# Optimization experiments

Hardware: AMD Instinct MI355X
Metric: run time of the kernel (lower is better)

The kernel has to match this reference:

```python
import jax, jax.numpy as jnp
import numpy as np

HIDDEN = 3072
N_HEADS = 16
Q_LORA = 1536
KV_LORA = 512
NOPE = 128
ROPE = 64
QK_HD = NOPE + ROPE  # 192
V_HD = 128
B, S = 2, 1024


def rms_norm(x, w, eps=1e-6):
    xf = x.astype(jnp.float32)
    var = jnp.mean(xf * xf, axis=-1, keepdims=True)
    return w * (xf * jax.lax.rsqrt(var + eps)).astype(x.dtype)


def apply_rope(x):
    # x: (b, s, h, d) with d even; interleaved pair rotation as in the source
    b, s, h, d = x.shape
    pos = jnp.arange(s, dtype=jnp.float32)
    inv_freq = 1.0 / (10000.0 ** (jnp.arange(0, d, 2, dtype=jnp.float32) / d))
    ang = pos[:, None] * inv_freq[None, :]          # (s, d/2)
    sin = jnp.sin(ang)[None, :, None, :]            # (1, s, 1, d/2)
    cos = jnp.cos(ang)[None, :, None, :]
    xr = x.reshape(b, s, h, d // 2, 2)
    x1, x2 = xr[..., 0], xr[..., 1]
    r1 = x1 * cos - x2 * sin
    r2 = x1 * sin + x2 * cos
    return jnp.stack([r1, r2], axis=-1).reshape(b, s, h, d)


def setup_inputs() -> dict:
    key = jax.random.key(0)
    ks = jax.random.split(key, 16)
    sc = 0.02
    inp = {
        "hidden_states": jax.random.normal(ks[0], (B, S, HIDDEN), jnp.float32),
        # causal additive mask (s, t): 0 on/below diagonal, -1e9 above
        "mask": jnp.where(jnp.tril(jnp.ones((S, S), bool)), 0.0, -1e9).astype(jnp.float32),
        "wq_a_w": jax.random.normal(ks[1], (Q_LORA, HIDDEN), jnp.float32) * sc,
        "wq_a_b": jnp.zeros((Q_LORA,), jnp.float32),
        "q_norm_w": jnp.ones((Q_LORA,), jnp.float32),
        "wq_b_w": jax.random.normal(ks[2], (HIDDEN, Q_LORA), jnp.float32) * sc,
        "wq_b_b": jnp.zeros((HIDDEN,), jnp.float32),
        "wkv_a_w": jax.random.normal(ks[3], (KV_LORA + ROPE, HIDDEN), jnp.float32) * sc,
        "wkv_a_b": jnp.zeros((KV_LORA + ROPE,), jnp.float32),
        "kv_norm_w": jnp.ones((KV_LORA,), jnp.float32),
        "wkv_b_w": jax.random.normal(ks[4], (N_HEADS * (NOPE + V_HD), KV_LORA), jnp.float32) * sc,
        "wkv_b_b": jnp.zeros((N_HEADS * (NOPE + V_HD),), jnp.float32),
        "wo_w": jax.random.normal(ks[5], (HIDDEN, N_HEADS * V_HD), jnp.float32) * sc,
        "wo_b": jnp.zeros((HIDDEN,), jnp.float32),
    }
    return inp


def reference(hidden_states, mask, wq_a_w, wq_a_b, q_norm_w, wq_b_w, wq_b_b,
              wkv_a_w, wkv_a_b, kv_norm_w, wkv_b_w, wkv_b_b, wo_w, wo_b):
    b, s, _ = hidden_states.shape
    scale = QK_HD ** (-0.5)

    # low-rank Q projection
    q_lat = hidden_states @ wq_a_w.T + wq_a_b                  # (b,s,q_lora)
    q = rms_norm(q_lat, q_norm_w) @ wq_b_w.T + wq_b_b          # (b,s,hidden)
    q = q.reshape(b, s, N_HEADS, QK_HD)
    q_nope, q_rope = q[..., :NOPE], q[..., NOPE:]
    q_rope = apply_rope(q_rope)
    q = jnp.concatenate([q_nope, q_rope], axis=-1)             # (b,s,h,192)

    # low-rank KV projection with decoupled rope key
    kv = hidden_states @ wkv_a_w.T + wkv_a_b                   # (b,s,kv_lora+rope)
    kv_lat, k_rope = kv[..., :KV_LORA], kv[..., KV_LORA:]
    k_rope = apply_rope(k_rope[:, :, None, :])                 # (b,s,1,64)
    kv = rms_norm(kv_lat, kv_norm_w) @ wkv_b_w.T + wkv_b_b
    kv = kv.reshape(b, s, N_HEADS, NOPE + V_HD)
    k_nope, v = kv[..., :NOPE], kv[..., NOPE:]
    k = jnp.concatenate([k_nope, jnp.broadcast_to(k_rope, (b, s, N_HEADS, ROPE))], axis=-1)

    # naive full attention, fp32 softmax (as in source)
    scores = jnp.einsum('bshd,bthd->bsht', q, k) * scale       # (b,s,h,t)
    scores = scores + mask[None, :, None, :]
    p = jax.nn.softmax(scores.astype(jnp.float32), axis=-1)
    out = jnp.einsum('bsht,bthd->bshd', p, v)                  # (b,s,h,v_hd)
    out = out.reshape(b, s, N_HEADS * V_HD)
    return out @ wo_w.T + wo_b
```

## Files before the change

kernel.cpp:

```cpp
#include <hip/hip_runtime.h>
#include <stdint.h>
#include <stddef.h>

#define NHEADS 16
#define QLORA  1536
#define KVLORA 512
#define QKH    192
#define VH     128
#define BB     2
#define SS     1024
#define MROWS  (BB*SS)
#define HID    3072

typedef __attribute__((ext_vector_type(4))) float fx4;
typedef __attribute__((ext_vector_type(4))) short sx4;
typedef __attribute__((ext_vector_type(8))) short sx8;

__device__ __forceinline__ short f2bf(float f) {
  uint32_t u = __builtin_bit_cast(uint32_t, f);
  u = (u + 0x7fffu + ((u >> 16) & 1u)) >> 16;
  return (short)u;
}
__device__ __forceinline__ float bf2f(short s) {
  uint32_t u = ((uint32_t)(uint16_t)s) << 16;
  return __builtin_bit_cast(float, u);
}
__device__ __forceinline__ void gl_lds16(const void* g, void* l) {
  __builtin_amdgcn_global_load_lds((const __attribute__((address_space(1))) void*)g,
                                   (__attribute__((address_space(3))) void*)l, 16, 0, 0);
}
__device__ __forceinline__ sx8 ldfrag(const short* p) {
  sx4 lo = *(const sx4*)p;
  sx4 hi = *(const sx4*)(p + 16);
  sx8 r;
  r[0]=lo[0]; r[1]=lo[1]; r[2]=lo[2]; r[3]=lo[3];
  r[4]=hi[0]; r[5]=hi[1]; r[6]=hi[2]; r[7]=hi[3];
  return r;
}
__device__ __forceinline__ sx8 ldfrag_swz(const short* lds, int row, int rowShorts,
                                          int baseChunk, int g) {
  const int r7 = row & 7;
  const int gh = g >> 1, lo4 = (g & 1) * 4;
  int ch0 = baseChunk + gh;
  int ch1 = baseChunk + 2 + gh;
  ch0 = (ch0 & ~7) | ((ch0 & 7) ^ r7);
  ch1 = (ch1 & ~7) | ((ch1 & 7) ^ r7);
  const short* base = lds + row * rowShorts;
  sx4 a = *(const sx4*)(base + ch0 * 8 + lo4);
  sx4 b = *(const sx4*)(base + ch1 * 8 + lo4);
  sx8 r;
  r[0]=a[0]; r[1]=a[1]; r[2]=a[2]; r[3]=a[3];
  r[4]=b[0]; r[5]=b[1]; r[6]=b[2]; r[7]=b[3];
  return r;
}

struct CvtSeg { const float* src; short* dst; int n4; };
__global__ void k_cvt6(CvtSeg s0, CvtSeg s1, CvtSeg s2, CvtSeg s3, CvtSeg s4, CvtSeg s5) {
  const CvtSeg segs[6] = {s0, s1, s2, s3, s4, s5};
  const int stride = gridDim.x * blockDim.x;
  const int t0 = blockIdx.x * blockDim.x + threadIdx.x;
#pragma unroll
  for (int s = 0; s < 6; ++s) {
    const float* src = segs[s].src;
    short* dst = segs[s].dst;
    const int n4 = segs[s].n4;
    for (int i = t0; i < n4; i += stride) {
      fx4 v = *(const fx4*)(src + (size_t)i * 4);
      sx4 o;
      o[0] = f2bf(v[0]); o[1] = f2bf(v[1]); o[2] = f2bf(v[2]); o[3] = f2bf(v[3]);
      *(sx4*)(dst + (size_t)i * 4) = o;
    }
  }
}

__global__ void k_rope_tab(float* __restrict__ tab) {
  int i = blockIdx.x * blockDim.x + threadIdx.x;
  if (i >= SS * 32) return;
  int pos = i >> 5, fi = i & 31;
  float inv = powf(10000.0f, -(float)fi / 32.0f);
  float ang = (float)pos * inv;
  tab[i * 2]     = cosf(ang);
  tab[i * 2 + 1] = sinf(ang);
}

struct GemmProb {
  const short* A; const short* Bt; const float* bias; void* C;
  int N; int K;
};

template <int MFR, int SPLITK>
__global__ __launch_bounds__(256, 2)
void k_gemmS(GemmProb p0, GemmProb p1, int nblk0) {
  constexpr int TM = MFR * 32;
  constexpr int MT = 2048 / TM;
  int nwg = gridDim.x;
  int bid = (blockIdx.x % 8) * (nwg >> 3) + (blockIdx.x >> 3);
  const GemmProb p = (bid < nblk0) ? p0 : p1;
  int lb = (bid < nblk0) ? bid : bid - nblk0;
  const int N = p.N, K = p.K;
  const int NT = (N + 127) >> 7;
  const int tiles = MT * NT;
  const int tile = lb % tiles;
  const int pi = (SPLITK > 1) ? (lb / tiles) : 0;
  const int m0 = (tile % MT) * TM;
  const int n0 = (tile / MT) * 128;
  const int Kc = K / SPLITK;
  const int k0 = pi * Kc;

  __shared__ short As[TM * 64];
  __shared__ short Bs[128 * 64];
  const int tid  = threadIdx.x;
  const int lane = tid & 63;
  const int g    = lane >> 4;
  const int r16  = lane & 15;
  const int wave = tid >> 6;
  const int wm   = (wave >> 1) * (TM / 2);
  const int wn   = (wave & 1) * 64;

  fx4 acc[MFR][4] = {};

  for (int kk = k0; kk < k0 + Kc; kk += 64) {
#pragma unroll
    for (int i = 0; i < MFR; ++i) {
      int cc  = tid + 256 * i;
      int row = cc >> 3;
      int src = ((cc & 7) ^ (row & 7)) * 8;
      gl_lds16(p.A + (size_t)(m0 + row) * K + kk + src, &As[cc * 8]);
    }
#pragma unroll
    for (int i = 0; i < 4; ++i) {
      int cc  = tid + 256 * i;
      int row = cc >> 3;
      int src = ((cc & 7) ^ (row & 7)) * 8;
      int bn = n0 + row; if (bn > N - 1) bn = N - 1;
      gl_lds16(p.Bt + (size_t)bn * K + kk + src, &Bs[cc * 8]);
    }
    __syncthreads();

#pragma unroll
    for (int s = 0; s < 2; ++s) {
      sx8 bfv[4];
#pragma unroll
      for (int ni = 0; ni < 4; ++ni)
        bfv[ni] = ldfrag_swz(Bs, wn + ni * 16 + r16, 64, s * 4, g);
#pragma unroll
      for (int mi = 0; mi < MFR; ++mi) {
        sx8 af = ldfrag_swz(As, wm + mi * 16 + r16, 64, s * 4, g);
#pragma unroll
        for (int ni = 0; ni < 4; ++ni)
          acc[mi][ni] = __builtin_amdgcn_mfma_f32_16x16x32_bf16(af, bfv[ni], acc[mi][ni], 0, 0, 0);
      }
    }
    __syncthreads();
  }

  if (SPLITK > 1) {
    float* Cp = (float*)p.C + (size_t)pi * 2048 * N;
#pragma unroll
    for (int mi = 0; mi < MFR; ++mi) {
      int mbase = m0 + wm + mi * 16 + 4 * g;
#pragma unroll
      for (int ni = 0; ni < 4; ++ni) {
        int ncol = n0 + wn + ni * 16 + r16;
        if (ncol < N) {
#pragma unroll
          for (int r = 0; r < 4; ++r)
            Cp[(size_t)(mbase + r) * N + ncol] = acc[mi][ni][r];
        }
      }
    }
  } else {
#pragma unroll
    for (int mi = 0; mi < MFR; ++mi) {
      int mbase = m0 + wm + mi * 16 + 4 * g;
#pragma unroll
      for (int ni = 0; ni < 4; ++ni) {
        int ncol = n0 + wn + ni * 16 + r16;
        if (ncol < N) {
          float bv = p.bias[ncol];
#pragma unroll
          for (int r = 0; r < 4; ++r)
            ((short*)p.C)[(size_t)(mbase + r) * N + ncol] = f2bf(acc[mi][ni][r] + bv);
        }
      }
    }
  }
}

__global__ __launch_bounds__(256)
void k_prep(const float* __restrict__ qp, const float* __restrict__ q_bias,
            const float* __restrict__ q_norm_w, short* __restrict__ qn,
            const float* __restrict__ kvp, const float* __restrict__ kv_bias,
            const float* __restrict__ kv_norm_w, short* __restrict__ kvn,
            short* __restrict__ kr, const float* __restrict__ tab) {
  const int row = blockIdx.x;
  const int t = threadIdx.x;
  const size_t QS = (size_t)2048 * QLORA;
  const size_t KS = (size_t)2048 * 576;

  float x[8];
  float s1 = 0.f, s2 = 0.f;
  if (t < 192) {
    const float* a = qp + (size_t)row * QLORA + t * 8;
    fx4 u0 = *(const fx4*)(a),          u1 = *(const fx4*)(a + 4);
    fx4 v0 = *(const fx4*)(a + QS),     v1 = *(const fx4*)(a + QS + 4);
    fx4 w0 = *(const fx4*)(a + 2 * QS), w1 = *(const fx4*)(a + 2 * QS + 4);
#pragma unroll
    for (int j = 0; j < 4; ++j) {
      x[j]     = u0[j] + v0[j] + w0[j] + q_bias[t * 8 + j];
      x[4 + j] = u1[j] + v1[j] + w1[j] + q_bias[t * 8 + 4 + j];
    }
#pragma unroll
    for (int j = 0; j < 8; ++j) s1 += x[j] * x[j];
  } else {
    const int c = t - 192;
    const float* a = kvp + (size_t)row * 576 + c * 8;
    fx4 u0 = *(const fx4*)(a),          u1 = *(const fx4*)(a + 4);
    fx4 v0 = *(const fx4*)(a + KS),     v1 = *(const fx4*)(a + KS + 4);
    fx4 w0 = *(const fx4*)(a + 2 * KS), w1 = *(const fx4*)(a + 2 * KS + 4);
#pragma unroll
    for (int j = 0; j < 4; ++j) {
      x[j]     = u0[j] + v0[j] + w0[j] + kv_bias[c * 8 + j];
      x[4 + j] = u1[j] + v1[j] + w1[j] + kv_bias[c * 8 + 4 + j];
    }
#pragma unroll
    for (int j = 0; j < 8; ++j) s2 += x[j] * x[j];
  }
#pragma unroll
  for (int o = 32; o >= 1; o >>= 1) {
    s1 += __shfl_xor(s1, o, 64);
    s2 += __shfl_xor(s2, o, 64);
  }
  __shared__ float r1[4], r2[4];
  if ((t & 63) == 0) { r1[t >> 6] = s1; r2[t >> 6] = s2; }
  __syncthreads();
  float qss = r1[0] + r1[1] + r1[2] + r1[3];
  float kss = r2[0] + r2[1] + r2[2] + r2[3];
  float qrs = 1.0f / sqrtf(qss / (float)QLORA + 1e-6f);
  float krs = 1.0f / sqrtf(kss / (float)KVLORA + 1e-6f);

  if (t < 192) {
    sx8 o;
#pragma unroll
    for (int j = 0; j < 8; ++j) o[j] = f2bf(x[j] * qrs * q_norm_w[t * 8 + j]);
    *(sx8*)(qn + (size_t)row * QLORA + t * 8) = o;
  } else {
    int c = t - 192;
    sx8 o;
#pragma unroll
    for (int j = 0; j < 8; ++j) o[j] = f2bf(x[j] * krs * kv_norm_w[c * 8 + j]);
    *(sx8*)(kvn + (size_t)row * KVLORA + c * 8) = o;
  }
  if (t < 8) {
    const float* a = kvp + (size_t)row * 576 + 512 + t * 8;
    fx4 u0 = *(const fx4*)(a),          u1 = *(const fx4*)(a + 4);
    fx4 v0 = *(const fx4*)(a + KS),     v1 = *(const fx4*)(a + KS + 4);
    fx4 w0 = *(const fx4*)(a + 2 * KS), w1 = *(const fx4*)(a + 2 * KS + 4);
    float y[8];
#pragma unroll
    for (int j = 0; j < 4; ++j) {
      y[j]     = u0[j] + v0[j] + w0[j] + kv_bias[512 + t * 8 + j];
      y[4 + j] = u1[j] + v1[j] + w1[j] + kv_bias[512 + t * 8 + 4 + j];
    }
    int pos = row & (SS - 1);
    sx8 o;
#pragma unroll
    for (int k = 0; k < 4; ++k) {
      int i = t * 4 + k;
      float c = tab[(pos * 32 + i) * 2], s = tab[(pos * 32 + i) * 2 + 1];
      o[2 * k]     = f2bf(y[2 * k] * c - y[2 * k + 1] * s);
      o[2 * k + 1] = f2bf(y[2 * k] * s + y[2 * k + 1] * c);
    }
    *(sx8*)(kr + (size_t)row * 64 + t * 8) = o;
  }
}

__global__ __launch_bounds__(256)
void k_post(const short* __restrict__ kvb, short* __restrict__ vt,
            short* __restrict__ qb, const float* __restrict__ tab) {
  const int bid = blockIdx.x;
  const int tid = threadIdx.x;
  if (bid < 512) {
    const int bh = bid >> 4;
    const int t0 = (bid & 15) * 64;
    const int b = bh >> 4, h = bh & 15;
    __shared__ short sm[64 * 128];
#pragma unroll
    for (int i = 0; i < 4; ++i) {
      int c = tid + 256 * i;
      int tt = c >> 4, d0 = (c & 15) * 8;
      sx8 v = *(const sx8*)(kvb + ((size_t)(b * SS + t0 + tt)) * 4096 + h * 256 + 128 + d0);
      *(sx8*)(sm + tt * 128 + d0) = v;
    }
    __syncthreads();
#pragma unroll
    for (int i = 0; i < 4; ++i) {
      int c = tid + 256 * i;
      int d = c >> 3, tof = (c & 7) * 8;
      sx8 v;
#pragma unroll
      for (int j = 0; j < 8; ++j) v[j] = sm[(tof + j) * 128 + d];
      *(sx8*)(vt + ((size_t)bh * VH + d) * SS + t0 + tof) = v;
    }
  } else {
    int p = (bid - 512) * 256 + tid;
    int j = p & 7, h = (p >> 3) & 15, row = p >> 7;
    int pos = row & (SS - 1);
    size_t base = (((size_t)row * NHEADS + h) * QKH) + 128 + j * 8;
    sx8 x = *(const sx8*)(qb + base);
    sx8 o;
#pragma unroll
    for (int k = 0; k < 4; ++k) {
      int i = j * 4 + k;
      float c = tab[(pos * 32 + i) * 2], s = tab[(pos * 32 + i) * 2 + 1];
      float x1 = bf2f(x[2 * k]), x2 = bf2f(x[2 * k + 1]);
      o[2 * k]     = f2bf(x1 * c - x2 * s);
      o[2 * k + 1] = f2bf(x1 * s + x2 * c);
    }
    *(sx8*)(qb + base) = o;
  }
}

__global__ __launch_bounds__(256)
void k_osum(const float* __restrict__ p, const float* __restrict__ bias,
            float* __restrict__ out) {
  const size_t OS = (size_t)2048 * HID;
  int i = blockIdx.x * 256 + threadIdx.x;
  fx4 a = *(const fx4*)(p + (size_t)i * 4);
  fx4 b = *(const fx4*)(p + OS + (size_t)i * 4);
  int col = (i * 4) % HID;
  fx4 bv = *(const fx4*)(bias + col);
  fx4 o = a + b + bv;
  *(fx4*)(out + (size_t)i * 4) = o;
}

__global__ __launch_bounds__(256, 2)
void k_attn(const short* __restrict__ q, const short* __restrict__ kvb,
            const short* __restrict__ kr, const short* __restrict__ vt,
            short* __restrict__ ao) {
  const int bh = blockIdx.x;
  const int b = bh >> 4, h = bh & 15;
  const int qt0 = blockIdx.y * 64;
  const int tid = threadIdx.x;
  const int lane = tid & 63;
  const int wave = tid >> 6;
  const int g = lane >> 4, r16 = lane & 15;
  const int qg = qt0 + wave * 16 + r16;

  __shared__ short Ks[64 * QKH];
  __shared__ short Vs[VH * 64];

  sx8 qf[6];
  {
    const short* qr = q + (((size_t)(b * SS + qg)) * NHEADS + h) * QKH;
#pragma unroll
    for (int f = 0; f < 6; ++f) qf[f] = ldfrag(qr + f * 32 + 4 * g);
  }

  float mrun = -1e30f, lrun = 0.0f;
  fx4 oacc[8] = {};
  const float scale = 0.07216878364870323f;

  const int ntiles = qt0 / 64 + 1;
  for (int kt = 0; kt < ntiles; ++kt) {
    const int t0 = kt * 64;
#pragma unroll
    for (int i = 0; i < 6; ++i) {
      int cc = tid + 256 * i;
      int row = cc / 24, ch = cc % 24;
      int sc = (ch & 24) | ((ch & 7) ^ (row & 7));
      size_t grow = (size_t)(b * SS + t0 + row);
      const short* src = (sc < 16) ? kvb + grow * 4096 + h * 256 + sc * 8
                                   : kr + grow * 64 + (sc - 16) * 8;
      gl_lds16(src, &Ks[cc * 8]);
    }
#pragma unroll
    for (int i = 0; i < 4; ++i) {
      int cc = tid + 256 * i;
      int row = cc >> 3;
      int sc = (cc & 7) ^ (row & 7);
      gl_lds16(vt + ((size_t)bh * VH + row) * SS + t0 + sc * 8, &Vs[cc * 8]);
    }
    __syncthreads();

    const bool diag = (kt == ntiles - 1);
    float pv[16];
    float tmax = -1e30f;
#pragma unroll
    for (int th = 0; th < 4; ++th) {
      fx4 sacc = {};
#pragma unroll
      for (int f = 0; f < 6; ++f) {
        sx8 kf = ldfrag_swz(Ks, th * 16 + r16, QKH, f * 4, g);
        sacc = __builtin_amdgcn_mfma_f32_16x16x32_bf16(kf, qf[f], sacc, 0, 0, 0);
      }
#pragma unroll
      for (int r = 0; r < 4; ++r) {
        int t = t0 + th * 16 + 4 * g + r;
        float s = sacc[r] * scale;
        if (diag && t > qg) s = -1e30f;
        pv[th * 4 + r] = s;
        tmax = fmaxf(tmax, s);
      }
    }
    tmax = fmaxf(tmax, __shfl_xor(tmax, 16, 64));
    tmax = fmaxf(tmax, __shfl_xor(tmax, 32, 64));
    float mnew = fmaxf(mrun, tmax);
    float corr = __expf(mrun - mnew);
    float psum = 0.f;
#pragma unroll
    for (int j = 0; j < 16; ++j) { pv[j] = __expf(pv[j] - mnew); psum += pv[j]; }
    psum += __shfl_xor(psum, 16, 64);
    psum += __shfl_xor(psum, 32, 64);
    lrun = lrun * corr + psum;
    mrun = mnew;
#pragma unroll
    for (int f8 = 0; f8 < 8; ++f8) oacc[f8] *= corr;

    sx8 pf0, pf1;
#pragma unroll
    for (int j = 0; j < 8; ++j) { pf0[j] = f2bf(pv[j]); pf1[j] = f2bf(pv[8 + j]); }

#pragma unroll
    for (int f8 = 0; f8 < 8; ++f8) {
      sx8 v0 = ldfrag_swz(Vs, f8 * 16 + r16, 64, 0, g);
      sx8 v1 = ldfrag_swz(Vs, f8 * 16 + r16, 64, 4, g);
      oacc[f8] = __builtin_amdgcn_mfma_f32_16x16x32_bf16(v0, pf0, oacc[f8], 0, 0, 0);
      oacc[f8] = __builtin_amdgcn_mfma_f32_16x16x32_bf16(v1, pf1, oacc[f8], 0, 0, 0);
    }
    __syncthreads();
  }

  float inv = 1.0f / lrun;
#pragma unroll
  for (int f8 = 0; f8 < 8; ++f8)
#pragma unroll
    for (int r = 0; r < 4; ++r) {
      int d = f8 * 16 + 4 * g + r;
      ao[(((size_t)(b * SS + qg)) * NHEADS + h) * VH + d] = f2bf(oacc[f8][r] * inv);
    }
}

extern "C" void kernel_launch(void* const* d_in, const int* in_sizes, int n_in,
                              void* d_out, int out_size, void* d_ws, size_t ws_size,
                              hipStream_t stream) {
  const float* hs       = (const float*)d_in[0];
  const float* wq_a_w   = (const float*)d_in[2];
  const float* wq_a_b   = (const float*)d_in[3];
  const float* q_norm_w = (const float*)d_in[4];
  const float* wq_b_w   = (const float*)d_in[5];
  const float* wq_b_b   = (const float*)d_in[6];
  const float* wkv_a_w  = (const float*)d_in[7];
  const float* wkv_a_b  = (const float*)d_in[8];
  const float* kv_norm_w= (const float*)d_in[9];
  const float* wkv_b_w  = (const float*)d_in[10];
  const float* wkv_b_b  = (const float*)d_in[11];
  const float* wo_w     = (const float*)d_in[12];
  const float* wo_b     = (const float*)d_in[13];
  float* out = (float*)d_out;

  short* ws0 = (short*)d_ws;
  size_t off = 0;
  short* wqa_bf  = ws0 + off; off += (size_t)QLORA * HID;
  short* wqb_bf  = ws0 + off; off += (size_t)HID * QLORA;
  short* wkva_bf = ws0 + off; off += (size_t)576 * HID;
  short* wkvb_bf = ws0 + off; off += (size_t)4096 * KVLORA;
  short* wo_bf   = ws0 + off; off += (size_t)HID * 2048;
  short* h_bf    = ws0 + off; off += (size_t)MROWS * HID;
  short* qn      = ws0 + off; off += (size_t)MROWS * QLORA;
  short* kvn     = ws0 + off; off += (size_t)MROWS * KVLORA;
  short* kr      = ws0 + off; off += (size_t)MROWS * 64;
  short* qb      = ws0 + off; off += (size_t)MROWS * HID;
  short* kvb     = ws0 + off; off += (size_t)MROWS * 4096;
  short* vtb     = ws0 + off; off += (size_t)BB * NHEADS * VH * SS;
  short* ao      = ws0 + off; off += (size_t)MROWS * 2048;
  float* tab     = (float*)(ws0 + off + (off & 1));
  float* arena   = tab + SS * 64;
  float* qlatp   = arena;
  float* kvp     = arena + (size_t)3 * 2048 * QLORA;
  float* wop     = arena;

  {
    CvtSeg s0{wq_a_w,  wqa_bf,  (int)((size_t)QLORA * HID / 4)};
    CvtSeg s1{wq_b_w,  wqb_bf,  (int)((size_t)HID * QLORA / 4)};
    CvtSeg s2{wkv_a_w, wkva_bf, (int)((size_t)576 * HID / 4)};
    CvtSeg s3{wkv_b_w, wkvb_bf, (int)((size_t)4096 * KVLORA / 4)};
    CvtSeg s4{wo_w,    wo_bf,   (int)((size_t)HID * 2048 / 4)};
    CvtSeg s5{hs,      h_bf,    (int)((size_t)MROWS * HID / 4)};
    k_cvt6<<<2048, 256, 0, stream>>>(s0, s1, s2, s3, s4, s5);
  }
  k_rope_tab<<<(SS * 32 + 255) / 256, 256, 0, stream>>>(tab);

  {
    GemmProb pq{h_bf, wqa_bf,  nullptr, qlatp, QLORA, HID};
    GemmProb pk{h_bf, wkva_bf, nullptr, kvp,   576,   HID};
    int nb0 = 8 * (QLORA / 128) * 3;
    int nb1 = 8 * ((576 + 127) / 128) * 3;
    k_gemmS<8, 3><<<nb0 + nb1, 256, 0, stream>>>(pq, pk, nb0);
  }

  k_prep<<<MROWS, 256, 0, stream>>>(qlatp, wq_a_b, q_norm_w, qn,
                                    kvp, wkv_a_b, kv_norm_w, kvn, kr, tab);

  {
    GemmProb pq{qn,  wqb_bf,  wq_b_b,  qb,  HID,  QLORA};
    GemmProb pk{kvn, wkvb_bf, wkv_b_b, kvb, 4096, KVLORA};
    int nb0 = 8 * (HID / 128);
    int nb1 = 8 * (4096 / 128);
    k_gemmS<8, 1><<<nb0 + nb1, 256, 0, stream>>>(pq, pk, nb0);
  }

  k_post<<<512 + 1024, 256, 0, stream>>>(kvb, vtb, qb, tab);

  k_attn<<<dim3(BB * NHEADS, SS / 64), 256, 0, stream>>>(qb, kvb, kr, vtb, ao);

  {
    GemmProb po{ao, wo_bf, nullptr, wop, HID, 2048};
    int nb = 8 * (HID / 128) * 2;
    k_gemmS<8, 2><<<nb, 256, 0, stream>>>(po, po, nb);
  }
  k_osum<<<(MROWS * HID / 4) / 256, 256, 0, stream>>>(wop, wo_b, out);
}
```

Measured before the change: 244.1 us.

## Overlap weight conversion with GEMMs, bf16 split-K partials, balance causal attention tiles

The conversion kernel now handles only the hidden states and the first-stage weights, and it also builds the rope table, which removes one launch. The remaining weight conversions run in 192 extra blocks appended to the earlier GEMM launches, so they overlap with matrix work. Split-K partial sums are stored as bf16 instead of fp32, halving partial-sum traffic at some cost in accuracy. The attention query-tile order is remapped to pair short and long causal tiles for better load balance.

```diff
diff --git a/kernel.cpp b/kernel.cpp
--- a/kernel.cpp
+++ b/kernel.cpp
@@ -55,32 +55,31 @@
 }
 
 struct CvtSeg { const float* src; short* dst; int n4; };
-__global__ void k_cvt6(CvtSeg s0, CvtSeg s1, CvtSeg s2, CvtSeg s3, CvtSeg s4, CvtSeg s5) {
-  const CvtSeg segs[6] = {s0, s1, s2, s3, s4, s5};
-  const int stride = gridDim.x * blockDim.x;
-  const int t0 = blockIdx.x * blockDim.x + threadIdx.x;
-#pragma unroll
-  for (int s = 0; s < 6; ++s) {
-    const float* src = segs[s].src;
-    short* dst = segs[s].dst;
-    const int n4 = segs[s].n4;
-    for (int i = t0; i < n4; i += stride) {
-      fx4 v = *(const fx4*)(src + (size_t)i * 4);
-      sx4 o;
-      o[0] = f2bf(v[0]); o[1] = f2bf(v[1]); o[2] = f2bf(v[2]); o[3] = f2bf(v[3]);
-      *(sx4*)(dst + (size_t)i * 4) = o;
-    }
-  }
-}
-
-__global__ void k_rope_tab(float* __restrict__ tab) {
-  int i = blockIdx.x * blockDim.x + threadIdx.x;
-  if (i >= SS * 32) return;
-  int pos = i >> 5, fi = i & 31;
-  float inv = powf(10000.0f, -(float)fi / 32.0f);
-  float ang = (float)pos * inv;
-  tab[i * 2]     = cosf(ang);
-  tab[i * 2 + 1] = sinf(ang);
+__device__ __forceinline__ void cvt_one(const CvtSeg& sg, int i) {
+  fx4 v = *(const fx4*)(sg.src + (size_t)i * 4);
+  sx4 o;
+  o[0] = f2bf(v[0]); o[1] = f2bf(v[1]); o[2] = f2bf(v[2]); o[3] = f2bf(v[3]);
+  *(sx4*)(sg.dst + (size_t)i * 4) = o;
+}
+
+__global__ void k_cvt3(CvtSeg s0, CvtSeg s1, CvtSeg s2, float* __restrict__ tab) {
+  if ((int)blockIdx.x >= 1024) {
+    int i = ((int)blockIdx.x - 1024) * 256 + threadIdx.x;
+    if (i < SS * 32) {
+      int pos = i >> 5, fi = i & 31;
+      float inv = powf(10000.0f, -(float)fi / 32.0f);
+      float ang = (float)pos * inv;
+      tab[i * 2]     = cosf(ang);
+      tab[i * 2 + 1] = sinf(ang);
+    }
+    return;
+  }
+  const CvtSeg segs[3] = {s0, s1, s2};
+  const int stride = 1024 * 256;
+  const int t0 = blockIdx.x * 256 + threadIdx.x;
+#pragma unroll
+  for (int s = 0; s < 3; ++s)
+    for (int i = t0; i < segs[s].n4; i += stride) cvt_one(segs[s], i);
 }
 
 struct GemmProb {
@@ -90,11 +89,18 @@
 
 template <int MFR, int SPLITK>
 __global__ __launch_bounds__(256, 2)
-void k_gemmS(GemmProb p0, GemmProb p1, int nblk0) {
+void k_gemmS(GemmProb p0, GemmProb p1, int nblk0, int nbGemm,
+             CvtSeg c0, CvtSeg c1) {
+  if ((int)blockIdx.x >= nbGemm) {
+    const int nthr = ((int)gridDim.x - nbGemm) * 256;
+    const int t0 = ((int)blockIdx.x - nbGemm) * 256 + threadIdx.x;
+    if (c0.src) for (int i = t0; i < c0.n4; i += nthr) cvt_one(c0, i);
+    if (c1.src) for (int i = t0; i < c1.n4; i += nthr) cvt_one(c1, i);
+    return;
+  }
   constexpr int TM = MFR * 32;
   constexpr int MT = 2048 / TM;
-  int nwg = gridDim.x;
-  int bid = (blockIdx.x % 8) * (nwg >> 3) + (blockIdx.x >> 3);
+  int bid = ((int)blockIdx.x % 8) * (nbGemm >> 3) + ((int)blockIdx.x >> 3);
   const GemmProb p = (bid < nblk0) ? p0 : p1;
   int lb = (bid < nblk0) ? bid : bid - nblk0;
   const int N = p.N, K = p.K;
@@ -155,7 +161,7 @@
   }
 
   if (SPLITK > 1) {
-    float* Cp = (float*)p.C + (size_t)pi * 2048 * N;
+    short* Cp = (short*)p.C + (size_t)pi * 2048 * N;
 #pragma unroll
     for (int mi = 0; mi < MFR; ++mi) {
       int mbase = m0 + wm + mi * 16 + 4 * g;
@@ -165,7 +171,7 @@
         if (ncol < N) {
 #pragma unroll
           for (int r = 0; r < 4; ++r)
-            Cp[(size_t)(mbase + r) * N + ncol] = acc[mi][ni][r];
+            Cp[(size_t)(mbase + r) * N + ncol] = f2bf(acc[mi][ni][r]);
         }
       }
     }
@@ -188,9 +194,9 @@
 }
 
 __global__ __launch_bounds__(256)
-void k_prep(const float* __restrict__ qp, const float* __restrict__ q_bias,
+void k_prep(const short* __restrict__ qp, const float* __restrict__ q_bias,
             const float* __restrict__ q_norm_w, short* __restrict__ qn,
-            const float* __restrict__ kvp, const float* __restrict__ kv_bias,
+            const short* __restrict__ kvp, const float* __restrict__ kv_bias,
             const float* __restrict__ kv_norm_w, short* __restrict__ kvn,
             short* __restrict__ kr, const float* __restrict__ tab) {
   const int row = blockIdx.x;
@@ -201,30 +207,26 @@
   float x[8];
   float s1 = 0.f, s2 = 0.f;
   if (t < 192) {
-    const float* a = qp + (size_t)row * QLORA + t * 8;
-    fx4 u0 = *(const fx4*)(a),          u1 = *(const fx4*)(a + 4);
-    fx4 v0 = *(const fx4*)(a + QS),     v1 = *(const fx4*)(a + QS + 4);
-    fx4 w0 = *(const fx4*)(a + 2 * QS), w1 = *(const fx4*)(a + 2 * QS + 4);
-#pragma unroll
-    for (int j = 0; j < 4; ++j) {
-      x[j]     = u0[j] + v0[j] + w0[j] + q_bias[t * 8 + j];
-      x[4 + j] = u1[j] + v1[j] + w1[j] + q_bias[t * 8 + 4 + j];
-    }
-#pragma unroll
-    for (int j = 0; j < 8; ++j) s1 += x[j] * x[j];
+    const short* a = qp + (size_t)row * QLORA + t * 8;
+    sx8 u = *(const sx8*)(a);
+    sx8 v = *(const sx8*)(a + QS);
+    sx8 w = *(const sx8*)(a + 2 * QS);
+#pragma unroll
+    for (int j = 0; j < 8; ++j) {
+      x[j] = bf2f(u[j]) + bf2f(v[j]) + bf2f(w[j]) + q_bias[t * 8 + j];
+      s1 += x[j] * x[j];
+    }
   } else {
     const int c = t - 192;
-    const float* a = kvp + (size_t)row * 576 + c * 8;
-    fx4 u0 = *(const fx4*)(a),          u1 = *(const fx4*)(a + 4);
-    fx4 v0 = *(const fx4*)(a + KS),     v1 = *(const fx4*)(a + KS + 4);
-    fx4 w0 = *(const fx4*)(a + 2 * KS), w1 = *(const fx4*)(a + 2 * KS + 4);
-#pragma unroll
-    for (int j = 0; j < 4; ++j) {
-      x[j]     = u0[j] + v0[j] + w0[j] + kv_bias[c * 8 + j];
-      x[4 + j] = u1[j] + v1[j] + w1[j] + kv_bias[c * 8 + 4 + j];
-    }
-#pragma unroll
-    for (int j = 0; j < 8; ++j) s2 += x[j] * x[j];
+    const short* a = kvp + (size_t)row * 576 + c * 8;
+    sx8 u = *(const sx8*)(a);
+    sx8 v = *(const sx8*)(a + KS);
+    sx8 w = *(const sx8*)(a + 2 * KS);
+#pragma unroll
+    for (int j = 0; j < 8; ++j) {
+      x[j] = bf2f(u[j]) + bf2f(v[j]) + bf2f(w[j]) + kv_bias[c * 8 + j];
+      s2 += x[j] * x[j];
+    }
   }
 #pragma unroll
   for (int o = 32; o >= 1; o >>= 1) {
@@ -252,16 +254,14 @@
     *(sx8*)(kvn + (size_t)row * KVLORA + c * 8) = o;
   }
   if (t < 8) {
-    const float* a = kvp + (size_t)row * 576 + 512 + t * 8;
-    fx4 u0 = *(const fx4*)(a),          u1 = *(const fx4*)(a + 4);
-    fx4 v0 = *(const fx4*)(a + KS),     v1 = *(const fx4*)(a + KS + 4);
-    fx4 w0 = *(const fx4*)(a + 2 * KS), w1 = *(const fx4*)(a + 2 * KS + 4);
+    const short* a = kvp + (size_t)row * 576 + 512 + t * 8;
+    sx8 u = *(const sx8*)(a);
+    sx8 v = *(const sx8*)(a + KS);
+    sx8 w = *(const sx8*)(a + 2 * KS);
     float y[8];
 #pragma unroll
-    for (int j = 0; j < 4; ++j) {
-      y[j]     = u0[j] + v0[j] + w0[j] + kv_bias[512 + t * 8 + j];
-      y[4 + j] = u1[j] + v1[j] + w1[j] + kv_bias[512 + t * 8 + 4 + j];
-    }
+    for (int j = 0; j < 8; ++j)
+      y[j] = bf2f(u[j]) + bf2f(v[j]) + bf2f(w[j]) + kv_bias[512 + t * 8 + j];
     int pos = row & (SS - 1);
     sx8 o;
 #pragma unroll
@@ -322,16 +322,21 @@
 }
 
 __global__ __launch_bounds__(256)
-void k_osum(const float* __restrict__ p, const float* __restrict__ bias,
+void k_osum(const short* __restrict__ p, const float* __restrict__ bias,
             float* __restrict__ out) {
   const size_t OS = (size_t)2048 * HID;
   int i = blockIdx.x * 256 + threadIdx.x;
-  fx4 a = *(const fx4*)(p + (size_t)i * 4);
-  fx4 b = *(const fx4*)(p + OS + (size_t)i * 4);
-  int col = (i * 4) % HID;
-  fx4 bv = *(const fx4*)(bias + col);
-  fx4 o = a + b + bv;
-  *(fx4*)(out + (size_t)i * 4) = o;
+  sx8 a = *(const sx8*)(p + (size_t)i * 8);
+  sx8 b = *(const sx8*)(p + OS + (size_t)i * 8);
+  int col = (i * 8) % HID;
+  fx4 o0, o1;
+#pragma unroll
+  for (int j = 0; j < 4; ++j) {
+    o0[j] = bf2f(a[j]) + bf2f(b[j]) + bias[col + j];
+    o1[j] = bf2f(a[4 + j]) + bf2f(b[4 + j]) + bias[col + 4 + j];
+  }
+  *(fx4*)(out + (size_t)i * 8) = o0;
+  *(fx4*)(out + (size_t)i * 8 + 4) = o1;
 }
 
 __global__ __launch_bounds__(256, 2)
@@ -340,7 +345,9 @@
             short* __restrict__ ao) {
   const int bh = blockIdx.x;
   const int b = bh >> 4, h = bh & 15;
-  const int qt0 = blockIdx.y * 64;
+  const int py = blockIdx.y;
+  const int qi = (py < 8) ? py : 23 - py;
+  const int qt0 = qi * 64;
   const int tid = threadIdx.x;
   const int lane = tid & 63;
   const int wave = tid >> 6;
@@ -475,28 +482,27 @@
   short* vtb     = ws0 + off; off += (size_t)BB * NHEADS * VH * SS;
   short* ao      = ws0 + off; off += (size_t)MROWS * 2048;
   float* tab     = (float*)(ws0 + off + (off & 1));
-  float* arena   = tab + SS * 64;
-  float* qlatp   = arena;
-  float* kvp     = arena + (size_t)3 * 2048 * QLORA;
-  float* wop     = arena;
+  short* arena   = (short*)(tab + SS * 64);
+  short* qlatp   = arena;
+  short* kvp     = arena + (size_t)3 * 2048 * QLORA;
+  short* wop     = arena;
 
   {
-    CvtSeg s0{wq_a_w,  wqa_bf,  (int)((size_t)QLORA * HID / 4)};
-    CvtSeg s1{wq_b_w,  wqb_bf,  (int)((size_t)HID * QLORA / 4)};
+    CvtSeg s0{hs,      h_bf,    (int)((size_t)MROWS * HID / 4)};
+    CvtSeg s1{wq_a_w,  wqa_bf,  (int)((size_t)QLORA * HID / 4)};
     CvtSeg s2{wkv_a_w, wkva_bf, (int)((size_t)576 * HID / 4)};
-    CvtSeg s3{wkv_b_w, wkvb_bf, (int)((size_t)4096 * KVLORA / 4)};
-    CvtSeg s4{wo_w,    wo_bf,   (int)((size_t)HID * 2048 / 4)};
-    CvtSeg s5{hs,      h_bf,    (int)((size_t)MROWS * HID / 4)};
-    k_cvt6<<<2048, 256, 0, stream>>>(s0, s1, s2, s3, s4, s5);
-  }
-  k_rope_tab<<<(SS * 32 + 255) / 256, 256, 0, stream>>>(tab);
+    k_cvt3<<<1024 + 128, 256, 0, stream>>>(s0, s1, s2, tab);
+  }
 
   {
     GemmProb pq{h_bf, wqa_bf,  nullptr, qlatp, QLORA, HID};
     GemmProb pk{h_bf, wkva_bf, nullptr, kvp,   576,   HID};
     int nb0 = 8 * (QLORA / 128) * 3;
     int nb1 = 8 * ((576 + 127) / 128) * 3;
-    k_gemmS<8, 3><<<nb0 + nb1, 256, 0, stream>>>(pq, pk, nb0);
+    int nbG = nb0 + nb1;
+    CvtSeg c0{wq_b_w,  wqb_bf,  (int)((size_t)HID * QLORA / 4)};
+    CvtSeg c1{wkv_b_w, wkvb_bf, (int)((size_t)4096 * KVLORA / 4)};
+    k_gemmS<8, 3><<<nbG + 192, 256, 0, stream>>>(pq, pk, nb0, nbG, c0, c1);
   }
 
   k_prep<<<MROWS, 256, 0, stream>>>(qlatp, wq_a_b, q_norm_w, qn,
@@ -507,7 +513,10 @@
     GemmProb pk{kvn, wkvb_bf, wkv_b_b, kvb, 4096, KVLORA};
     int nb0 = 8 * (HID / 128);
     int nb1 = 8 * (4096 / 128);
-    k_gemmS<8, 1><<<nb0 + nb1, 256, 0, stream>>>(pq, pk, nb0);
+    int nbG = nb0 + nb1;
+    CvtSeg c0{wo_w, wo_bf, (int)((size_t)HID * 2048 / 4)};
+    CvtSeg c1{nullptr, nullptr, 0};
+    k_gemmS<8, 1><<<nbG + 192, 256, 0, stream>>>(pq, pk, nb0, nbG, c0, c1);
   }
 
   k_post<<<512 + 1024, 256, 0, stream>>>(kvb, vtb, qb, tab);
@@ -517,7 +526,8 @@
   {
     GemmProb po{ao, wo_bf, nullptr, wop, HID, 2048};
     int nb = 8 * (HID / 128) * 2;
-    k_gemmS<8, 2><<<nb, 256, 0, stream>>>(po, po, nb);
-  }
-  k_osum<<<(MROWS * HID / 4) / 256, 256, 0, stream>>>(wop, wo_b, out);
-}
+    CvtSeg cz{nullptr, nullptr, 0};
+    k_gemmS<8, 2><<<nb, 256, 0, stream>>>(po, po, nb, nb, cz, cz);
+  }
+  k_osum<<<(MROWS * HID / 8) / 256, 256, 0, stream>>>(wop, wo_b, out);
+}
```

Result: faster. 230.8 us, median of 3 (-5.4%).
